# Optimization experiments

Hardware: AMD Instinct MI355X
Metric: run time of the kernel (lower is better)

Reference implementation:

```python
import jax, jax.numpy as jnp
import numpy as np
import math

D_MODEL = 1024
N_HEADS = 16
D_KV = 64
INNER = N_HEADS * D_KV
NUM_BUCKETS = 32
MAX_DISTANCE = 128


def _relative_position_bucket(relative_position, bidirectional=True,
                              num_buckets=NUM_BUCKETS, max_distance=MAX_DISTANCE):
    # faithful port of T5Attention._relative_position_bucket
    relative_buckets = jnp.zeros_like(relative_position)
    if bidirectional:
        num_buckets //= 2
        relative_buckets = relative_buckets + (relative_position > 0).astype(jnp.int32) * num_buckets
        relative_position = jnp.abs(relative_position)
    else:
        relative_position = -jnp.minimum(relative_position, jnp.zeros_like(relative_position))
    max_exact = num_buckets // 2
    is_small = relative_position < max_exact
    rp_large = max_exact + (
        jnp.log(relative_position.astype(jnp.float32) / max_exact)
        / math.log(max_distance / max_exact) * (num_buckets - max_exact)
    ).astype(jnp.int32)
    rp_large = jnp.minimum(rp_large, num_buckets - 1)
    return relative_buckets + jnp.where(is_small, relative_position, rp_large)


def compute_bias(rel_bias_table, q_len, k_len):
    # [q_len, k_len] relative positions -> bucket ids -> [1, H, q_len, k_len] bias
    context = jnp.arange(q_len, dtype=jnp.int32)[:, None]
    memory = jnp.arange(k_len, dtype=jnp.int32)[None, :]
    buckets = _relative_position_bucket(memory - context, bidirectional=True)
    values = rel_bias_table[buckets]            # [q, k, H]
    return jnp.transpose(values, (2, 0, 1))[None]  # [1, H, q, k]


def setup_inputs() -> dict:
    key = jax.random.key(0)
    ks = jax.random.split(key, 6)
    B, S = 2, 2048
    scale = 0.02
    return {
        "hidden_states": jax.random.normal(ks[0], (B, S, D_MODEL), jnp.float32),
        # weights stored as [in, out] (torch Linear applies x @ W.T with W [out,in])
        "w_q": jax.random.normal(ks[1], (D_MODEL, INNER), jnp.float32) * scale,
        "w_k": jax.random.normal(ks[2], (D_MODEL, INNER), jnp.float32) * scale,
        "w_v": jax.random.normal(ks[3], (D_MODEL, INNER), jnp.float32) * scale,
        "w_o": jax.random.normal(ks[4], (INNER, D_MODEL), jnp.float32) * scale,
        "rel_bias_table": jax.random.normal(ks[5], (NUM_BUCKETS, N_HEADS), jnp.float32) * scale,
    }


def reference(hidden_states, w_q, w_k, w_v, w_o, rel_bias_table):
    B, S, _ = hidden_states.shape

    def shape(x):  # [B, S, inner] -> [B, H, S, d_kv]
        return jnp.transpose(x.reshape(B, S, N_HEADS, D_KV), (0, 2, 1, 3))

    q = shape(hidden_states @ w_q)  # note: T5 applies no 1/sqrt(d) scaling
    k = shape(hidden_states @ w_k)
    v = shape(hidden_states @ w_v)

    scores = jnp.einsum("bhqd,bhkd->bhqk", q, k)
    position_bias = compute_bias(rel_bias_table, S, S)
    scores = scores + position_bias
    attn = jax.nn.softmax(scores.astype(jnp.float32), axis=-1).astype(scores.dtype)
    ctx = jnp.einsum("bhqk,bhkd->bhqd", attn, v)
    ctx = jnp.transpose(ctx, (0, 2, 1, 3)).reshape(B, S, INNER)
    return ctx @ w_o
```

## Files before the change

kernel.cpp:

```cpp
#include <hip/hip_runtime.h>
#include <math.h>

#define S_LEN 2048
#define DM 1024

typedef __attribute__((ext_vector_type(8))) __bf16 bf16x8;
typedef __attribute__((ext_vector_type(4))) float floatx4;

typedef __attribute__((address_space(1))) const unsigned int g_u32;
typedef __attribute__((address_space(3))) unsigned int l_u32;

__device__ __forceinline__ unsigned short f2bf(float f) {
  union { float f; unsigned int u; } v; v.f = f;
  return (unsigned short)((v.u + 0x7fffu + ((v.u >> 16) & 1u)) >> 16);
}
__device__ __forceinline__ float bf2f(unsigned short u) {
  union { unsigned int u; float f; } v; v.u = ((unsigned int)u) << 16;
  return v.f;
}
__device__ __forceinline__ bf16x8 ld_frag(const unsigned short* p) {
  union { uint4 u; bf16x8 v; } t;
  t.u = *(const uint4*)p;
  return t.v;
}

__global__ void detect_k(const unsigned short* __restrict__ x, int* __restrict__ flag) {
  __shared__ int cnt;
  if (threadIdx.x == 0) cnt = 0;
  __syncthreads();
  int local = 0;
  for (int i = threadIdx.x; i < 4096; i += 256) {
    unsigned short u = x[i];
    int e = (u >> 7) & 0xFF;
    if (e > 140) local++;
  }
  atomicAdd(&cnt, local);
  __syncthreads();
  if (threadIdx.x == 0) *flag = (cnt > 64) ? 1 : 0;
}

__global__ void conv_x(const void* __restrict__ src, unsigned short* __restrict__ dst,
                       const int* __restrict__ flag, int n8) {
  int i = blockIdx.x * 256 + threadIdx.x;
  if (i >= n8) return;
  if (*flag) {
    const float4* s = (const float4*)src;
    float4 a = s[2 * i], b = s[2 * i + 1];
    union { uint4 u4; unsigned short s[8]; } o;
    o.s[0] = f2bf(a.x); o.s[1] = f2bf(a.y); o.s[2] = f2bf(a.z); o.s[3] = f2bf(a.w);
    o.s[4] = f2bf(b.x); o.s[5] = f2bf(b.y); o.s[6] = f2bf(b.z); o.s[7] = f2bf(b.w);
    ((uint4*)dst)[i] = o.u4;
  } else {
    ((uint4*)dst)[i] = ((const uint4*)src)[i];
  }
}

__global__ void transpose_w(const void* __restrict__ s0, const void* __restrict__ s1,
                            const void* __restrict__ s2, const void* __restrict__ s3,
                            unsigned short* __restrict__ Wcat, unsigned short* __restrict__ Wto,
                            const int* __restrict__ flag) {
  __shared__ float tile[32][33];
  const int z = blockIdx.z;
  const void* src = (z == 0) ? s0 : (z == 1) ? s1 : (z == 2) ? s2 : s3;
  unsigned short* dst = (z < 3) ? (Wcat + (size_t)z * 1048576) : Wto;
  const int isf = *flag;
  int x = blockIdx.x * 32 + threadIdx.x;
  int y0 = blockIdx.y * 32;
  for (int i = threadIdx.y; i < 32; i += 8) {
    float v;
    if (isf) v = ((const float*)src)[(size_t)(y0 + i) * DM + x];
    else     v = bf2f(((const unsigned short*)src)[(size_t)(y0 + i) * DM + x]);
    tile[i][threadIdx.x] = v;
  }
  __syncthreads();
  int xo = y0 + threadIdx.x;
  for (int i = threadIdx.y; i < 32; i += 8)
    dst[(size_t)(blockIdx.x * 32 + i) * DM + xo] = f2bf(tile[threadIdx.x][i]);
}

__global__ void bias_k(const void* __restrict__ table, float* __restrict__ out,
                       const int* __restrict__ flag) {
  int idx = blockIdx.x * 256 + threadIdx.x;
  if (idx >= 16 * 4095) return;
  int h = idx / 4095;
  int j = idx - h * 4095;
  int delta = j - 2047;
  int bucket = (delta > 0) ? 16 : 0;
  int ad = (delta < 0) ? -delta : delta;
  int smallv;
  if (ad < 8) smallv = ad;
  else {
    int l = (int)(log((double)ad * 0.125) * (8.0 / log(16.0)));
    smallv = 8 + l;
    if (smallv > 15) smallv = 15;
  }
  bucket += smallv;
  float v;
  if (*flag) v = ((const float*)table)[bucket * 16 + h];
  else       v = bf2f(((const unsigned short*)table)[bucket * 16 + h]);
  out[idx] = v;
}

__global__ __launch_bounds__(256) void gemm_bt(
    const unsigned short* __restrict__ A, const unsigned short* __restrict__ Bt,
    void* __restrict__ C, int mode, const int* __restrict__ flag)
{
  __shared__ __align__(16) unsigned short smem[128 * 136];
  unsigned short* As = smem;
  unsigned short* Bs = smem + 8192;
  const int tid = threadIdx.x;
  const int lane = tid & 63, wave = tid >> 6;
  const int l16 = lane & 15, quad = lane >> 4;
  const int wm = (wave >> 1) << 6, wn = (wave & 1) << 6;
  const int m0 = blockIdx.y << 7, n0 = blockIdx.x << 7;
  const int lrow = lane >> 3, lcol = (lane & 7) << 3;

  floatx4 acc[4][4] = {};

  for (int k0 = 0; k0 < 1024; k0 += 64) {
    __syncthreads();
#pragma unroll
    for (int i = 0; i < 4; ++i) {
      int r0 = wave * 32 + i * 8;
      __builtin_amdgcn_global_load_lds(
          (g_u32*)(const void*)(A + (size_t)(m0 + r0 + lrow) * 1024 + k0 + lcol),
          (l_u32*)(void*)&As[r0 * 64], 16, 0, 0);
      __builtin_amdgcn_global_load_lds(
          (g_u32*)(const void*)(Bt + (size_t)(n0 + r0 + lrow) * 1024 + k0 + lcol),
          (l_u32*)(void*)&Bs[r0 * 64], 16, 0, 0);
    }
    __syncthreads();
#pragma unroll
    for (int ks = 0; ks < 2; ++ks) {
      bf16x8 a[4], b[4];
#pragma unroll
      for (int mi = 0; mi < 4; ++mi)
        a[mi] = *(const bf16x8*)&As[(wm + mi * 16 + l16) * 64 + ks * 32 + quad * 8];
#pragma unroll
      for (int ni = 0; ni < 4; ++ni)
        b[ni] = *(const bf16x8*)&Bs[(wn + ni * 16 + l16) * 64 + ks * 32 + quad * 8];
#pragma unroll
      for (int mi = 0; mi < 4; ++mi)
#pragma unroll
        for (int ni = 0; ni < 4; ++ni)
          acc[mi][ni] = __builtin_amdgcn_mfma_f32_16x16x32_bf16(a[mi], b[ni], acc[mi][ni], 0, 0, 0);
    }
  }

  if (mode == 0) {
    unsigned short* Cs = (unsigned short*)C;
    const int mat = n0 >> 10;
    if (mat < 2) {
#pragma unroll
      for (int mi = 0; mi < 4; ++mi)
#pragma unroll
        for (int ni = 0; ni < 4; ++ni)
#pragma unroll
          for (int i = 0; i < 4; ++i) {
            int m = m0 + wm + mi * 16 + quad * 4 + i;
            int n = (n0 & 1023) + wn + ni * 16 + l16;
            int b = m >> 11, s = m & 2047, h = n >> 6, d = n & 63;
            Cs[(size_t)mat * 4194304 + (((size_t)(b * 16 + h)) * 2048 + s) * 64 + d] =
                f2bf(acc[mi][ni][i]);
          }
    } else {
      __syncthreads();
#pragma unroll
      for (int mi = 0; mi < 4; ++mi)
#pragma unroll
        for (int ni = 0; ni < 4; ++ni) {
          union { unsigned short s[4]; uint2 u; } w;
#pragma unroll
          for (int i = 0; i < 4; ++i) w.s[i] = f2bf(acc[mi][ni][i]);
          *(uint2*)&smem[(wn + ni * 16 + l16) * 136 + wm + mi * 16 + quad * 4] = w.u;
        }
      __syncthreads();
      const int bb = m0 >> 11, s0 = m0 & 2047, nb = n0 & 1023;
#pragma unroll
      for (int it = 0; it < 8; ++it) {
        int r = it * 16 + (tid >> 4);
        int c = (tid & 15) * 8;
        uint4 rv = *(const uint4*)&smem[r * 136 + c];
        *(uint4*)&Cs[(size_t)2 * 4194304 + (size_t)(bb * 1024 + nb + r) * 2048 + s0 + c] = rv;
      }
    }
  } else {
    const int isf = *flag;
#pragma unroll
    for (int mi = 0; mi < 4; ++mi)
#pragma unroll
      for (int ni = 0; ni < 4; ++ni)
#pragma unroll
        for (int i = 0; i < 4; ++i) {
          int m = m0 + wm + mi * 16 + quad * 4 + i;
          int n = n0 + wn + ni * 16 + l16;
          size_t idx = (size_t)m * 1024 + n;
          float v = acc[mi][ni][i];
          if (isf) ((float*)C)[idx] = v;
          else     ((unsigned short*)C)[idx] = f2bf(v);
        }
  }
}

__global__ __launch_bounds__(256) void gemm_out(
    const unsigned short* __restrict__ A, const unsigned short* __restrict__ Bt,
    void* __restrict__ C, const int* __restrict__ flag)
{
  __shared__ __align__(16) unsigned short As[128 * 64];
  __shared__ __align__(16) unsigned short Bs[64 * 64];
  const int tid = threadIdx.x;
  const int lane = tid & 63, wave = tid >> 6;
  const int l16 = lane & 15, quad = lane >> 4;
  const int wm = (wave >> 1) << 6, wn = (wave & 1) << 5;
  const int m0 = blockIdx.y << 7, n0 = blockIdx.x << 6;
  const int lrow = lane >> 3, lcol = (lane & 7) << 3;

  floatx4 acc[4][2] = {};

  for (int k0 = 0; k0 < 1024; k0 += 64) {
    __syncthreads();
#pragma unroll
    for (int i = 0; i < 4; ++i) {
      int r0 = wave * 32 + i * 8;
      __builtin_amdgcn_global_load_lds(
          (g_u32*)(const void*)(A + (size_t)(m0 + r0 + lrow) * 1024 + k0 + lcol),
          (l_u32*)(void*)&As[r0 * 64], 16, 0, 0);
    }
#pragma unroll
    for (int i = 0; i < 2; ++i) {
      int r0 = wave * 16 + i * 8;
      __builtin_amdgcn_global_load_lds(
          (g_u32*)(const void*)(Bt + (size_t)(n0 + r0 + lrow) * 1024 + k0 + lcol),
          (l_u32*)(void*)&Bs[r0 * 64], 16, 0, 0);
    }
    __syncthreads();
#pragma unroll
    for (int ks = 0; ks < 2; ++ks) {
      bf16x8 a[4], b[2];
#pragma unroll
      for (int mi = 0; mi < 4; ++mi)
        a[mi] = *(const bf16x8*)&As[(wm + mi * 16 + l16) * 64 + ks * 32 + quad * 8];
#pragma unroll
      for (int ni = 0; ni < 2; ++ni)
        b[ni] = *(const bf16x8*)&Bs[(wn + ni * 16 + l16) * 64 + ks * 32 + quad * 8];
#pragma unroll
      for (int mi = 0; mi < 4; ++mi)
#pragma unroll
        for (int ni = 0; ni < 2; ++ni)
          acc[mi][ni] = __builtin_amdgcn_mfma_f32_16x16x32_bf16(a[mi], b[ni], acc[mi][ni], 0, 0, 0);
    }
  }

  const int isf = *flag;
#pragma unroll
  for (int mi = 0; mi < 4; ++mi)
#pragma unroll
    for (int ni = 0; ni < 2; ++ni)
#pragma unroll
      for (int i = 0; i < 4; ++i) {
        int m = m0 + wm + mi * 16 + quad * 4 + i;
        int n = n0 + wn + ni * 16 + l16;
        size_t idx = (size_t)m * 1024 + n;
        float v = acc[mi][ni][i];
        if (isf) ((float*)C)[idx] = v;
        else     ((unsigned short*)C)[idx] = f2bf(v);
      }
}

#define STAGE_KV(kv0, buf)                                                    \
  _Pragma("unroll")                                                           \
  for (int i = 0; i < 2; ++i) {                                               \
    int rr = i * 32 + wave * 8 + (lane >> 3);                                 \
    int sw = ((lane & 7) ^ (lane >> 3)) << 3;                                 \
    __builtin_amdgcn_global_load_lds(                                         \
        (g_u32*)(const void*)(Kp + (size_t)((kv0) + rr) * 64 + sw),           \
        (l_u32*)(void*)&Ks[buf][i * 2048 + wave * 512], 16, 0, 0);            \
    __builtin_amdgcn_global_load_lds(                                         \
        (g_u32*)(const void*)(Vp + (size_t)rr * S_LEN + (kv0) + sw),          \
        (l_u32*)(void*)&Vs[buf][i * 2048 + wave * 512], 16, 0, 0);            \
  }

__global__ __launch_bounds__(256, 2) void attn_k(
    const unsigned short* __restrict__ Q, const unsigned short* __restrict__ K,
    const unsigned short* __restrict__ Vt, const float* __restrict__ bias,
    unsigned short* __restrict__ ctx)
{
  __shared__ __align__(16) unsigned short Ks[2][4096];
  __shared__ __align__(16) unsigned short Vs[2][4096];
  __shared__ __align__(16) unsigned short Ps[4][32][72];
  __shared__ float Bls[2176];
  const int tid = threadIdx.x;
  const int lane = tid & 63, wave = tid >> 6;
  const int l16 = lane & 15, quad = lane >> 4;
  const int bh = blockIdx.y;
  const int b = bh >> 4, h = bh & 15;
  const int q0 = blockIdx.x << 7;
  const int wq = wave << 5;

  const unsigned short* Qp = Q + (size_t)bh * S_LEN * 64;
  const unsigned short* Kp = K + (size_t)bh * S_LEN * 64;
  const unsigned short* Vp = Vt + (size_t)bh * 64 * S_LEN;
  const float* biasg = bias + h * 4095 + (1920 - q0);

  STAGE_KV(0, 0);
  for (int i = tid; i < 2175; i += 256)
    Bls[i] = fmaf(biasg[i], 1.44269504f, -24.f);

  bf16x8 qf[2][2];
#pragma unroll
  for (int mi = 0; mi < 2; ++mi)
#pragma unroll
    for (int ks = 0; ks < 2; ++ks)
      qf[mi][ks] = ld_frag(Qp + (size_t)(q0 + wq + mi * 16 + l16) * 64 + ks * 32 + quad * 8);

  float l_run[2][4] = {};
  floatx4 oacc[2][4] = {};

  const int qwb = q0 + wq;
  const int rbase = 127 + l16 - wq - (quad << 2);

  __syncthreads();
  const float Bneg = Bls[0], Bpos = Bls[2174];

  for (int kv0 = 0; kv0 < S_LEN; kv0 += 64) {
    const int cur = (kv0 >> 6) & 1;
    if (kv0 + 64 < S_LEN) STAGE_KV(kv0 + 64, cur ^ 1);

    floatx4 sac[2][4] = {};
#pragma unroll
    for (int ks = 0; ks < 2; ++ks) {
      bf16x8 kf[4];
#pragma unroll
      for (int ni = 0; ni < 4; ++ni)
        kf[ni] = *(const bf16x8*)&Ks[cur][(ni * 16 + l16) * 64 +
                                          ((((ks << 2) + quad) ^ (l16 & 7)) << 3)];
#pragma unroll
      for (int mi = 0; mi < 2; ++mi)
#pragma unroll
        for (int ni = 0; ni < 4; ++ni)
          sac[mi][ni] = __builtin_amdgcn_mfma_f32_16x16x32_bf16(qf[mi][ks], kf[ni], sac[mi][ni], 0, 0, 0);
    }

    {
      const int dmin = kv0 - (qwb + 31);
      const int dmax = kv0 + 63 - qwb;
      if (dmin >= 96 || dmax <= -96) {
        const float bc = (dmin >= 96) ? Bpos : Bneg;
#pragma unroll
        for (int mi = 0; mi < 2; ++mi)
#pragma unroll
          for (int i = 0; i < 4; ++i) {
            float sum = 0.f;
#pragma unroll
            for (int ni = 0; ni < 4; ++ni) {
              float e = __builtin_amdgcn_exp2f(fmaf(sac[mi][ni][i], 1.44269504f, bc));
              sac[mi][ni][i] = e; sum += e;
            }
            l_run[mi][i] += sum;
          }
      } else {
#pragma unroll
        for (int mi = 0; mi < 2; ++mi)
#pragma unroll
          for (int i = 0; i < 4; ++i) {
            const int bbase = kv0 + rbase - i - mi * 16;
            float sum = 0.f;
#pragma unroll
            for (int ni = 0; ni < 4; ++ni) {
              float e = __builtin_amdgcn_exp2f(
                  fmaf(sac[mi][ni][i], 1.44269504f, Bls[bbase + ni * 16]));
              sac[mi][ni][i] = e; sum += e;
            }
            l_run[mi][i] += sum;
          }
      }
    }

#pragma unroll
    for (int mi = 0; mi < 2; ++mi)
#pragma unroll
      for (int ni = 0; ni < 4; ++ni)
#pragma unroll
        for (int i = 0; i < 4; ++i)
          Ps[wave][mi * 16 + quad * 4 + i][ni * 16 + l16] = f2bf(sac[mi][ni][i]);

#pragma unroll
    for (int ks2 = 0; ks2 < 2; ++ks2) {
      bf16x8 af[2], vf[4];
#pragma unroll
      for (int mi = 0; mi < 2; ++mi)
        af[mi] = *(const bf16x8*)&Ps[wave][mi * 16 + l16][ks2 * 32 + quad * 8];
#pragma unroll
      for (int ni = 0; ni < 4; ++ni)
        vf[ni] = *(const bf16x8*)&Vs[cur][(ni * 16 + l16) * 64 +
                                          ((((ks2 << 2) + quad) ^ (l16 & 7)) << 3)];
#pragma unroll
      for (int mi = 0; mi < 2; ++mi)
#pragma unroll
        for (int ni = 0; ni < 4; ++ni)
          oacc[mi][ni] = __builtin_amdgcn_mfma_f32_16x16x32_bf16(af[mi], vf[ni], oacc[mi][ni], 0, 0, 0);
    }

    __syncthreads();
  }

  float linv[2][4];
#pragma unroll
  for (int mi = 0; mi < 2; ++mi)
#pragma unroll
    for (int i = 0; i < 4; ++i) {
      float ls = l_run[mi][i];
      ls += __shfl_xor(ls, 1);
      ls += __shfl_xor(ls, 2);
      ls += __shfl_xor(ls, 4);
      ls += __shfl_xor(ls, 8);
      linv[mi][i] = 1.f / ls;
    }

#pragma unroll
  for (int mi = 0; mi < 2; ++mi)
#pragma unroll
    for (int ni = 0; ni < 4; ++ni)
#pragma unroll
      for (int i = 0; i < 4; ++i) {
        float v = oacc[mi][ni][i] * linv[mi][i];
        int srow = q0 + wq + mi * 16 + quad * 4 + i;
        ctx[((size_t)(b * 2048 + srow)) * 1024 + h * 64 + ni * 16 + l16] = f2bf(v);
      }
}

extern "C" void kernel_launch(void* const* d_in, const int* in_sizes, int n_in,
                              void* d_out, int out_size, void* d_ws, size_t ws_size,
                              hipStream_t stream) {
  char* ws = (char*)d_ws;
  unsigned short* Xbf  = (unsigned short*)(ws);
  unsigned short* Wcat = (unsigned short*)(ws + 8388608);
  unsigned short* Wto  = (unsigned short*)(ws + 14680064);
  unsigned short* Qb   = (unsigned short*)(ws + 16777216);
  unsigned short* ctx  = (unsigned short*)(ws + 41943040);
  float*          bias = (float*)(ws + 50331648);
  int*            flag = (int*)(ws + 50593792);

  unsigned short* Kb  = Qb + 4194304;
  unsigned short* Vtb = Qb + 8388608;

  detect_k<<<1, 256, 0, stream>>>((const unsigned short*)d_in[0], flag);
  conv_x<<<2048, 256, 0, stream>>>(d_in[0], Xbf, flag, 524288);
  transpose_w<<<dim3(32, 32, 4), dim3(32, 8), 0, stream>>>(
      d_in[1], d_in[2], d_in[3], d_in[4], Wcat, Wto, flag);
  bias_k<<<256, 256, 0, stream>>>(d_in[5], bias, flag);

  gemm_bt<<<dim3(24, 32), 256, 0, stream>>>(Xbf, Wcat, Qb, 0, flag);

  attn_k<<<dim3(16, 32), 256, 0, stream>>>(Qb, Kb, Vtb, bias, ctx);

  gemm_out<<<dim3(16, 32), 256, 0, stream>>>(ctx, Wto, d_out, flag);
}
```

Measured before the change: 230.9 us.

## Halve attention query tile, shrink bias table, fuse bias build into conversion

The attention kernel now gives each block 64 query rows (16 per wave) instead of 128, which doubles the grid to 1024 blocks and cuts per-wave registers and LDS. The relative-bias table is reduced to a 384-entry window per head holding only the near-diagonal values, pre-scaled by log2(e) with the -24 offset. It is built inside the X conversion kernel, removing one launch. The cost is that each block reloads K/V for half as many queries, doubling total K/V traffic, and each MFMA pass reuses the K/V fragments across fewer rows.

```diff
diff --git a/kernel.cpp b/kernel.cpp
--- a/kernel.cpp
+++ b/kernel.cpp
@@ -39,19 +39,42 @@
   if (threadIdx.x == 0) *flag = (cnt > 64) ? 1 : 0;
 }
 
-__global__ void conv_x(const void* __restrict__ src, unsigned short* __restrict__ dst,
-                       const int* __restrict__ flag, int n8) {
-  int i = blockIdx.x * 256 + threadIdx.x;
-  if (i >= n8) return;
-  if (*flag) {
-    const float4* s = (const float4*)src;
-    float4 a = s[2 * i], b = s[2 * i + 1];
-    union { uint4 u4; unsigned short s[8]; } o;
-    o.s[0] = f2bf(a.x); o.s[1] = f2bf(a.y); o.s[2] = f2bf(a.z); o.s[3] = f2bf(a.w);
-    o.s[4] = f2bf(b.x); o.s[5] = f2bf(b.y); o.s[6] = f2bf(b.z); o.s[7] = f2bf(b.w);
-    ((uint4*)dst)[i] = o.u4;
+__global__ void conv_bias(const void* __restrict__ src, unsigned short* __restrict__ dst,
+                          const void* __restrict__ table, float* __restrict__ outb,
+                          const int* __restrict__ flag) {
+  const int bid = blockIdx.x, tid = threadIdx.x;
+  if (bid < 2048) {
+    int i = bid * 256 + tid;
+    if (*flag) {
+      const float4* s = (const float4*)src;
+      float4 a = s[2 * i], b = s[2 * i + 1];
+      union { uint4 u4; unsigned short s[8]; } o;
+      o.s[0] = f2bf(a.x); o.s[1] = f2bf(a.y); o.s[2] = f2bf(a.z); o.s[3] = f2bf(a.w);
+      o.s[4] = f2bf(b.x); o.s[5] = f2bf(b.y); o.s[6] = f2bf(b.z); o.s[7] = f2bf(b.w);
+      ((uint4*)dst)[i] = o.u4;
+    } else {
+      ((uint4*)dst)[i] = ((const uint4*)src)[i];
+    }
   } else {
-    ((uint4*)dst)[i] = ((const uint4*)src)[i];
+    int idx = (bid - 2048) * 256 + tid;
+    if (idx >= 16 * 384) return;
+    int h = idx / 384;
+    int j = idx - h * 384;
+    int delta = j - 192;
+    int bucket = (delta > 0) ? 16 : 0;
+    int ad = (delta < 0) ? -delta : delta;
+    int smallv;
+    if (ad < 8) smallv = ad;
+    else {
+      int l = (int)(log((double)ad * 0.125) * (8.0 / log(16.0)));
+      smallv = 8 + l;
+      if (smallv > 15) smallv = 15;
+    }
+    bucket += smallv;
+    float v;
+    if (*flag) v = ((const float*)table)[bucket * 16 + h];
+    else       v = bf2f(((const unsigned short*)table)[bucket * 16 + h]);
+    outb[idx] = v * 1.44269504f - 24.f;
   }
 }
 
@@ -78,32 +101,9 @@
     dst[(size_t)(blockIdx.x * 32 + i) * DM + xo] = f2bf(tile[threadIdx.x][i]);
 }
 
-__global__ void bias_k(const void* __restrict__ table, float* __restrict__ out,
-                       const int* __restrict__ flag) {
-  int idx = blockIdx.x * 256 + threadIdx.x;
-  if (idx >= 16 * 4095) return;
-  int h = idx / 4095;
-  int j = idx - h * 4095;
-  int delta = j - 2047;
-  int bucket = (delta > 0) ? 16 : 0;
-  int ad = (delta < 0) ? -delta : delta;
-  int smallv;
-  if (ad < 8) smallv = ad;
-  else {
-    int l = (int)(log((double)ad * 0.125) * (8.0 / log(16.0)));
-    smallv = 8 + l;
-    if (smallv > 15) smallv = 15;
-  }
-  bucket += smallv;
-  float v;
-  if (*flag) v = ((const float*)table)[bucket * 16 + h];
-  else       v = bf2f(((const unsigned short*)table)[bucket * 16 + h]);
-  out[idx] = v;
-}
-
 __global__ __launch_bounds__(256) void gemm_bt(
     const unsigned short* __restrict__ A, const unsigned short* __restrict__ Bt,
-    void* __restrict__ C, int mode, const int* __restrict__ flag)
+    void* __restrict__ C)
 {
   __shared__ __align__(16) unsigned short smem[128 * 136];
   unsigned short* As = smem;
@@ -147,45 +147,9 @@
     }
   }
 
-  if (mode == 0) {
-    unsigned short* Cs = (unsigned short*)C;
-    const int mat = n0 >> 10;
-    if (mat < 2) {
-#pragma unroll
-      for (int mi = 0; mi < 4; ++mi)
-#pragma unroll
-        for (int ni = 0; ni < 4; ++ni)
-#pragma unroll
-          for (int i = 0; i < 4; ++i) {
-            int m = m0 + wm + mi * 16 + quad * 4 + i;
-            int n = (n0 & 1023) + wn + ni * 16 + l16;
-            int b = m >> 11, s = m & 2047, h = n >> 6, d = n & 63;
-            Cs[(size_t)mat * 4194304 + (((size_t)(b * 16 + h)) * 2048 + s) * 64 + d] =
-                f2bf(acc[mi][ni][i]);
-          }
-    } else {
-      __syncthreads();
-#pragma unroll
-      for (int mi = 0; mi < 4; ++mi)
-#pragma unroll
-        for (int ni = 0; ni < 4; ++ni) {
-          union { unsigned short s[4]; uint2 u; } w;
-#pragma unroll
-          for (int i = 0; i < 4; ++i) w.s[i] = f2bf(acc[mi][ni][i]);
-          *(uint2*)&smem[(wn + ni * 16 + l16) * 136 + wm + mi * 16 + quad * 4] = w.u;
-        }
-      __syncthreads();
-      const int bb = m0 >> 11, s0 = m0 & 2047, nb = n0 & 1023;
-#pragma unroll
-      for (int it = 0; it < 8; ++it) {
-        int r = it * 16 + (tid >> 4);
-        int c = (tid & 15) * 8;
-        uint4 rv = *(const uint4*)&smem[r * 136 + c];
-        *(uint4*)&Cs[(size_t)2 * 4194304 + (size_t)(bb * 1024 + nb + r) * 2048 + s0 + c] = rv;
-      }
-    }
-  } else {
-    const int isf = *flag;
+  unsigned short* Cs = (unsigned short*)C;
+  const int mat = n0 >> 10;
+  if (mat < 2) {
 #pragma unroll
     for (int mi = 0; mi < 4; ++mi)
 #pragma unroll
@@ -193,12 +157,31 @@
 #pragma unroll
         for (int i = 0; i < 4; ++i) {
           int m = m0 + wm + mi * 16 + quad * 4 + i;
-          int n = n0 + wn + ni * 16 + l16;
-          size_t idx = (size_t)m * 1024 + n;
-          float v = acc[mi][ni][i];
-          if (isf) ((float*)C)[idx] = v;
-          else     ((unsigned short*)C)[idx] = f2bf(v);
+          int n = (n0 & 1023) + wn + ni * 16 + l16;
+          int b = m >> 11, s = m & 2047, h = n >> 6, d = n & 63;
+          Cs[(size_t)mat * 4194304 + (((size_t)(b * 16 + h)) * 2048 + s) * 64 + d] =
+              f2bf(acc[mi][ni][i]);
         }
+  } else {
+    __syncthreads();
+#pragma unroll
+    for (int mi = 0; mi < 4; ++mi)
+#pragma unroll
+      for (int ni = 0; ni < 4; ++ni) {
+        union { unsigned short s[4]; uint2 u; } w;
+#pragma unroll
+        for (int i = 0; i < 4; ++i) w.s[i] = f2bf(acc[mi][ni][i]);
+        *(uint2*)&smem[(wn + ni * 16 + l16) * 136 + wm + mi * 16 + quad * 4] = w.u;
+      }
+    __syncthreads();
+    const int bb = m0 >> 11, s0 = m0 & 2047, nb = n0 & 1023;
+#pragma unroll
+    for (int it = 0; it < 8; ++it) {
+      int r = it * 16 + (tid >> 4);
+      int c = (tid & 15) * 8;
+      uint4 rv = *(const uint4*)&smem[r * 136 + c];
+      *(uint4*)&Cs[(size_t)2 * 4194304 + (size_t)(bb * 1024 + nb + r) * 2048 + s0 + c] = rv;
+    }
   }
 }
 
@@ -287,46 +270,43 @@
 {
   __shared__ __align__(16) unsigned short Ks[2][4096];
   __shared__ __align__(16) unsigned short Vs[2][4096];
-  __shared__ __align__(16) unsigned short Ps[4][32][72];
-  __shared__ float Bls[2176];
+  __shared__ __align__(16) unsigned short Ps[4][16][72];
+  __shared__ float Bls[384];
   const int tid = threadIdx.x;
   const int lane = tid & 63, wave = tid >> 6;
   const int l16 = lane & 15, quad = lane >> 4;
   const int bh = blockIdx.y;
   const int b = bh >> 4, h = bh & 15;
-  const int q0 = blockIdx.x << 7;
-  const int wq = wave << 5;
+  const int q0 = blockIdx.x << 6;
+  const int wq = wave << 4;
 
   const unsigned short* Qp = Q + (size_t)bh * S_LEN * 64;
   const unsigned short* Kp = K + (size_t)bh * S_LEN * 64;
   const unsigned short* Vp = Vt + (size_t)bh * 64 * S_LEN;
-  const float* biasg = bias + h * 4095 + (1920 - q0);
+  const float* biasg = bias + h * 384;
 
   STAGE_KV(0, 0);
-  for (int i = tid; i < 2175; i += 256)
-    Bls[i] = fmaf(biasg[i], 1.44269504f, -24.f);
-
-  bf16x8 qf[2][2];
-#pragma unroll
-  for (int mi = 0; mi < 2; ++mi)
-#pragma unroll
-    for (int ks = 0; ks < 2; ++ks)
-      qf[mi][ks] = ld_frag(Qp + (size_t)(q0 + wq + mi * 16 + l16) * 64 + ks * 32 + quad * 8);
-
-  float l_run[2][4] = {};
-  floatx4 oacc[2][4] = {};
+  for (int i = tid; i < 384; i += 256) Bls[i] = biasg[i];
+
+  bf16x8 qf[2];
+#pragma unroll
+  for (int ks = 0; ks < 2; ++ks)
+    qf[ks] = ld_frag(Qp + (size_t)(q0 + wq + l16) * 64 + ks * 32 + quad * 8);
+
+  float l_run[4] = {};
+  floatx4 oacc[4] = {};
 
   const int qwb = q0 + wq;
-  const int rbase = 127 + l16 - wq - (quad << 2);
+  const int rbase = 192 + l16 - (quad << 2) - qwb;
 
   __syncthreads();
-  const float Bneg = Bls[0], Bpos = Bls[2174];
+  const float Bneg = Bls[0], Bpos = Bls[383];
 
   for (int kv0 = 0; kv0 < S_LEN; kv0 += 64) {
     const int cur = (kv0 >> 6) & 1;
     if (kv0 + 64 < S_LEN) STAGE_KV(kv0 + 64, cur ^ 1);
 
-    floatx4 sac[2][4] = {};
+    floatx4 sac[4] = {};
 #pragma unroll
     for (int ks = 0; ks < 2; ++ks) {
       bf16x8 kf[4];
@@ -335,98 +315,82 @@
         kf[ni] = *(const bf16x8*)&Ks[cur][(ni * 16 + l16) * 64 +
                                           ((((ks << 2) + quad) ^ (l16 & 7)) << 3)];
 #pragma unroll
-      for (int mi = 0; mi < 2; ++mi)
-#pragma unroll
-        for (int ni = 0; ni < 4; ++ni)
-          sac[mi][ni] = __builtin_amdgcn_mfma_f32_16x16x32_bf16(qf[mi][ks], kf[ni], sac[mi][ni], 0, 0, 0);
+      for (int ni = 0; ni < 4; ++ni)
+        sac[ni] = __builtin_amdgcn_mfma_f32_16x16x32_bf16(qf[ks], kf[ni], sac[ni], 0, 0, 0);
     }
 
     {
-      const int dmin = kv0 - (qwb + 31);
+      const int dmin = kv0 - (qwb + 15);
       const int dmax = kv0 + 63 - qwb;
       if (dmin >= 96 || dmax <= -96) {
         const float bc = (dmin >= 96) ? Bpos : Bneg;
 #pragma unroll
-        for (int mi = 0; mi < 2; ++mi)
-#pragma unroll
-          for (int i = 0; i < 4; ++i) {
-            float sum = 0.f;
-#pragma unroll
-            for (int ni = 0; ni < 4; ++ni) {
-              float e = __builtin_amdgcn_exp2f(fmaf(sac[mi][ni][i], 1.44269504f, bc));
-              sac[mi][ni][i] = e; sum += e;
-            }
-            l_run[mi][i] += sum;
+        for (int i = 0; i < 4; ++i) {
+          float sum = 0.f;
+#pragma unroll
+          for (int ni = 0; ni < 4; ++ni) {
+            float e = __builtin_amdgcn_exp2f(fmaf(sac[ni][i], 1.44269504f, bc));
+            sac[ni][i] = e; sum += e;
           }
+          l_run[i] += sum;
+        }
       } else {
 #pragma unroll
-        for (int mi = 0; mi < 2; ++mi)
-#pragma unroll
-          for (int i = 0; i < 4; ++i) {
-            const int bbase = kv0 + rbase - i - mi * 16;
-            float sum = 0.f;
-#pragma unroll
-            for (int ni = 0; ni < 4; ++ni) {
-              float e = __builtin_amdgcn_exp2f(
-                  fmaf(sac[mi][ni][i], 1.44269504f, Bls[bbase + ni * 16]));
-              sac[mi][ni][i] = e; sum += e;
-            }
-            l_run[mi][i] += sum;
+        for (int i = 0; i < 4; ++i) {
+          const int bbase = kv0 + rbase - i;
+          float sum = 0.f;
+#pragma unroll
+          for (int ni = 0; ni < 4; ++ni) {
+            float e = __builtin_amdgcn_exp2f(
+                fmaf(sac[ni][i], 1.44269504f, Bls[bbase + ni * 16]));
+            sac[ni][i] = e; sum += e;
           }
+          l_run[i] += sum;
+        }
       }
     }
 
 #pragma unroll
-    for (int mi = 0; mi < 2; ++mi)
-#pragma unroll
-      for (int ni = 0; ni < 4; ++ni)
-#pragma unroll
-        for (int i = 0; i < 4; ++i)
-          Ps[wave][mi * 16 + quad * 4 + i][ni * 16 + l16] = f2bf(sac[mi][ni][i]);
+    for (int ni = 0; ni < 4; ++ni)
+#pragma unroll
+      for (int i = 0; i < 4; ++i)
+        Ps[wave][quad * 4 + i][ni * 16 + l16] = f2bf(sac[ni][i]);
 
 #pragma unroll
     for (int ks2 = 0; ks2 < 2; ++ks2) {
-      bf16x8 af[2], vf[4];
-#pragma unroll
-      for (int mi = 0; mi < 2; ++mi)
-        af[mi] = *(const bf16x8*)&Ps[wave][mi * 16 + l16][ks2 * 32 + quad * 8];
+      bf16x8 af, vf[4];
+      af = *(const bf16x8*)&Ps[wave][l16][ks2 * 32 + quad * 8];
 #pragma unroll
       for (int ni = 0; ni < 4; ++ni)
         vf[ni] = *(const bf16x8*)&Vs[cur][(ni * 16 + l16) * 64 +
                                           ((((ks2 << 2) + quad) ^ (l16 & 7)) << 3)];
 #pragma unroll
-      for (int mi = 0; mi < 2; ++mi)
-#pragma unroll
-        for (int ni = 0; ni < 4; ++ni)
-          oacc[mi][ni] = __builtin_amdgcn_mfma_f32_16x16x32_bf16(af[mi], vf[ni], oacc[mi][ni], 0, 0, 0);
-    }
-
-    __syncthreads();
-  }
-
-  float linv[2][4];
-#pragma unroll
-  for (int mi = 0; mi < 2; ++mi)
+      for (int ni = 0; ni < 4; ++ni)
+        oacc[ni] = __builtin_amdgcn_mfma_f32_16x16x32_bf16(af, vf[ni], oacc[ni], 0, 0, 0);
+    }
+
+    __syncthreads();
+  }
+
+  float linv[4];
+#pragma unroll
+  for (int i = 0; i < 4; ++i) {
+    float ls = l_run[i];
+    ls += __shfl_xor(ls, 1);
+    ls += __shfl_xor(ls, 2);
+    ls += __shfl_xor(ls, 4);
+    ls += __shfl_xor(ls, 8);
+    linv[i] = 1.f / ls;
+  }
+
+#pragma unroll
+  for (int ni = 0; ni < 4; ++ni)
 #pragma unroll
     for (int i = 0; i < 4; ++i) {
-      float ls = l_run[mi][i];
-      ls += __shfl_xor(ls, 1);
-      ls += __shfl_xor(ls, 2);
-      ls += __shfl_xor(ls, 4);
-      ls += __shfl_xor(ls, 8);
-      linv[mi][i] = 1.f / ls;
-    }
-
-#pragma unroll
-  for (int mi = 0; mi < 2; ++mi)
-#pragma unroll
-    for (int ni = 0; ni < 4; ++ni)
-#pragma unroll
-      for (int i = 0; i < 4; ++i) {
-        float v = oacc[mi][ni][i] * linv[mi][i];
-        int srow = q0 + wq + mi * 16 + quad * 4 + i;
-        ctx[((size_t)(b * 2048 + srow)) * 1024 + h * 64 + ni * 16 + l16] = f2bf(v);
-      }
+      float v = oacc[ni][i] * linv[i];
+      int srow = q0 + wq + quad * 4 + i;
+      ctx[((size_t)(b * 2048 + srow)) * 1024 + h * 64 + ni * 16 + l16] = f2bf(v);
+    }
 }
 
 extern "C" void kernel_launch(void* const* d_in, const int* in_sizes, int n_in,
@@ -445,14 +409,13 @@
   unsigned short* Vtb = Qb + 8388608;
 
   detect_k<<<1, 256, 0, stream>>>((const unsigned short*)d_in[0], flag);
-  conv_x<<<2048, 256, 0, stream>>>(d_in[0], Xbf, flag, 524288);
+  conv_bias<<<2072, 256, 0, stream>>>(d_in[0], Xbf, d_in[5], bias, flag);
   transpose_w<<<dim3(32, 32, 4), dim3(32, 8), 0, stream>>>(
       d_in[1], d_in[2], d_in[3], d_in[4], Wcat, Wto, flag);
-  bias_k<<<256, 256, 0, stream>>>(d_in[5], bias, flag);
-
-  gemm_bt<<<dim3(24, 32), 256, 0, stream>>>(Xbf, Wcat, Qb, 0, flag);
-
-  attn_k<<<dim3(16, 32), 256, 0, stream>>>(Qb, Kb, Vtb, bias, ctx);
+
+  gemm_bt<<<dim3(24, 32), 256, 0, stream>>>(Xbf, Wcat, Qb);
+
+  attn_k<<<dim3(32, 32), 256, 0, stream>>>(Qb, Kb, Vtb, bias, ctx);
 
   gemm_out<<<dim3(16, 32), 256, 0, stream>>>(ctx, Wto, d_out, flag);
 }
```

Measured after the change: 239.7 us. 1.04x slower.
